# Performance work log

Measured on AMD Instinct MI355X. Metric: run time of the kernel, lower is better.

The kernel has to match this reference:

```python
import jax, jax.numpy as jnp
import numpy as np

N, C, D = 131072, 512, 3


def setup_inputs() -> dict:
    key = jax.random.key(0)
    kx, kmu = jax.random.split(key)
    X = jax.random.normal(kx, (N, D), dtype=jnp.float32)
    mu = jax.random.normal(kmu, (C, D), dtype=jnp.float32)
    w = jnp.zeros((C,), dtype=jnp.float32)
    # sigma as in __init__: r = sqrt(sum of per-dim unbiased variances of mu0)
    r = jnp.sqrt(jnp.var(mu, axis=0, ddof=1).sum())
    sigma = (0.1 * (r / C ** (1.0 / D))).astype(jnp.float32)
    return {"X": X, "mu": mu, "w": w, "sigma": sigma}


def reference(X, mu, w, sigma):
    # One EM step of a uniform-covariance GMM (EM_step_pytorch).
    n, d = X.shape
    # pairwise squared distances [N, C]
    D2_nc = ((X[:, None, :] - mu[None, :, :]) ** 2).sum(-1)
    # log-responsibilities (E-step), softmax over components
    lgamma_nc = jax.nn.log_softmax(w[None, :] - D2_nc / (2.0 * sigma ** 2), axis=1)
    gamma_nc = jnp.exp(lgamma_nc)
    # M-step: centroids (softmax over points, per component)
    mu_new = jax.nn.softmax(lgamma_nc, axis=0).T @ X  # [C, D]
    # M-step: component scores
    h_c = jax.nn.logsumexp(lgamma_nc, axis=0)  # [C]
    w_new = h_c - h_c.mean()
    # M-step: uniform std
    sigma_new = jnp.sqrt((gamma_nc * D2_nc).sum() / (d * n))
    # EM values: expected targets and free energy
    Y = gamma_nc @ mu_new  # [N, D]
    logpi_c = w_new - jax.nn.logsumexp(w_new)
    Cfe = (gamma_nc * (
        ((mu_new ** 2).sum(-1)[None, :] - (Y ** 2).sum(-1)[:, None]) / (2.0 * sigma_new ** 2)
        + d * jnp.log(sigma_new)
        - logpi_c[None, :]
        + lgamma_nc
    )).sum()
    return Y, Cfe
```

## Files before the change

### kernel.cpp

```cpp
#include <hip/hip_runtime.h>
#include <cfloat>
#include <cmath>

#define NPTS 131072
#define NC   512
#define NREP 4
#define L2E  1.4426950408889634f
#define LN2  0.6931471805599453f
#define CUT  34.0f

#define PM4_OFF  0
#define PQ4_OFF  2048
#define ST4_OFF  4096
#define MISC_OFF 12288

__device__ __forceinline__ float waveSum(float v) {
#pragma unroll
  for (int off = 32; off > 0; off >>= 1) v += __shfl_down(v, off, 64);
  return v;
}
__device__ __forceinline__ float waveMax(float v) {
#pragma unroll
  for (int off = 32; off > 0; off >>= 1) v = fmaxf(v, __shfl_down(v, off, 64));
  return v;
}

__global__ __launch_bounds__(512) void k_prep(
    const float* __restrict__ mu, const float* __restrict__ w,
    const float* __restrict__ sigma, float4* __restrict__ pm,
    float* __restrict__ ST, float* __restrict__ misc) {
  const int t = threadIdx.x;
  const float sg = sigma[0];
  const float k2 = L2E / (2.0f * sg * sg);
  const float m0 = mu[3 * t], m1 = mu[3 * t + 1], m2 = mu[3 * t + 2];
  pm[t] = make_float4(2.0f * k2 * m0, 2.0f * k2 * m1, 2.0f * k2 * m2,
                      w[t] * L2E - (m0 * m0 + m1 * m1 + m2 * m2) * k2);
#pragma unroll
  for (int r = 0; r < NREP * 4; ++r) ST[r * 512 + t] = 0.f;
  if (t < 8) misc[t] = 0.f;
}

__global__ __launch_bounds__(512, 4) void k_estep(
    const float* __restrict__ X, const float4* __restrict__ pm,
    float* __restrict__ ST, float* __restrict__ misc,
    float* __restrict__ out) {
  __shared__ float  s_m[8][64];
  __shared__ float2 s_sq[8][64];
  __shared__ float  s_M[64];
  __shared__ float  s_z[64];
  __shared__ float4 s_acc[NC];

  const int t = threadIdx.x;
  const int p = t & 63;
  const int ch = __builtin_amdgcn_readfirstlane(t >> 6);
  const int n = blockIdx.x * 64 + p;
  const float x0 = X[3 * n], x1 = X[3 * n + 1], x2 = X[3 * n + 2];

  s_acc[t] = make_float4(0.f, 0.f, 0.f, 0.f);

  const float4* __restrict__ pmc = pm + ch * 64;
  float l[64];
  float ma = -FLT_MAX, mb = -FLT_MAX, mc2 = -FLT_MAX, md = -FLT_MAX;
#pragma unroll
  for (int i = 0; i < 64; i += 4) {
    float4 a = pmc[i], b = pmc[i + 1], c = pmc[i + 2], d = pmc[i + 3];
    l[i]     = fmaf(a.x, x0, fmaf(a.y, x1, fmaf(a.z, x2, a.w)));
    l[i + 1] = fmaf(b.x, x0, fmaf(b.y, x1, fmaf(b.z, x2, b.w)));
    l[i + 2] = fmaf(c.x, x0, fmaf(c.y, x1, fmaf(c.z, x2, c.w)));
    l[i + 3] = fmaf(d.x, x0, fmaf(d.y, x1, fmaf(d.z, x2, d.w)));
    ma  = fmaxf(ma, l[i]);      mb = fmaxf(mb, l[i + 1]);
    mc2 = fmaxf(mc2, l[i + 2]); md = fmaxf(md, l[i + 3]);
  }
  s_m[ch][p] = fmaxf(fmaxf(ma, mb), fmaxf(mc2, md));
  __syncthreads();

  if (t < 64) {
    float v = s_m[0][t];
#pragma unroll
    for (int c = 1; c < 8; ++c) v = fmaxf(v, s_m[c][t]);
    s_M[t] = v;
  }
  __syncthreads();

  const float M = s_M[p];
  const float thr = M - CUT;

  float sE = 0.f, qE = 0.f;
#pragma unroll
  for (int i = 0; i < 64; ++i) {
    if (l[i] >= thr) {
      const float d = l[i] - M;
      const float e = exp2f(d);
      sE += e;
      qE = fmaf(e, d, qE);
    }
  }
  s_sq[ch][p] = make_float2(sE, qE);
  __syncthreads();

  if (t < 64) {
    float ss = 0.f, qq = 0.f;
#pragma unroll
    for (int c = 0; c < 8; ++c) { float2 v = s_sq[c][t]; ss += v.x; qq += v.y; }
    const float lg = __log2f(ss);
    const float z = s_M[t] + lg;
    s_z[t] = z;
    out[3 * n] = z;
    const float La = LN2 * (__fdividef(qq, ss) - lg);
    const float xx = x0 * x0 + x1 * x1 + x2 * x2;
    const float rl = waveSum(La);
    const float rx = waveSum(xx);
    if (t == 0) { atomicAdd(&misc[3], rl); atomicAdd(&misc[0], rx); }
  }
  __syncthreads();

  const float z = s_z[p];
#pragma unroll
  for (int i = 0; i < 64; ++i) {
    if (l[i] >= thr) {
      const float g = exp2f(l[i] - z);
      float* a = (float*)(s_acc + (ch * 64 + i));
      atomicAdd(a + 0, g * x0);
      atomicAdd(a + 1, g * x1);
      atomicAdd(a + 2, g * x2);
      atomicAdd(a + 3, g);
    }
  }
  __syncthreads();

  float4 v = s_acc[t];
  if (v.w != 0.f) {
    float* st = ST + (((blockIdx.x & (NREP - 1)) * 512 + t) << 2);
    atomicAdd(st + 0, v.x);
    atomicAdd(st + 1, v.y);
    atomicAdd(st + 2, v.z);
    atomicAdd(st + 3, v.w);
  }
}

__global__ __launch_bounds__(512) void k_mstep(
    const float* __restrict__ mu, const float4* __restrict__ ST4,
    float4* __restrict__ pq, float* __restrict__ misc,
    float* __restrict__ out) {
  __shared__ float s_red[8];
  __shared__ float s_red2[8];
  __shared__ float s_bc[4];
  const int t = threadIdx.x;

  float Tx = 0.f, Ty = 0.f, Tz = 0.f, S = 0.f;
#pragma unroll
  for (int r = 0; r < NREP; ++r) {
    float4 v = ST4[r * 512 + t];
    Tx += v.x; Ty += v.y; Tz += v.z; S += v.w;
  }
  const float Sc = fmaxf(S, 1e-30f);
  const float h = __logf(Sc);
  const float m0 = Tx / Sc, m1 = Ty / Sc, m2 = Tz / Sc;

  const float o0 = mu[3 * t], o1 = mu[3 * t + 1], o2 = mu[3 * t + 2];
  const float gdp = S * (o0 * o0 + o1 * o1 + o2 * o2)
                    - 2.0f * (o0 * Tx + o1 * Ty + o2 * Tz);

  float hm = waveMax(h);
  if ((t & 63) == 0) s_red[t >> 6] = hm;
  __syncthreads();
  if (t == 0) {
    float v = s_red[0];
    for (int i = 1; i < 8; ++i) v = fmaxf(v, s_red[i]);
    s_bc[0] = v;
  }
  __syncthreads();
  const float hM = s_bc[0];

  float es = waveSum(__expf(h - hM));
  float gs = waveSum(gdp);
  if ((t & 63) == 0) { s_red[t >> 6] = es; s_red2[t >> 6] = gs; }
  __syncthreads();
  if (t == 0) {
    float esum = 0.f, gsum = 0.f;
    for (int i = 0; i < 8; ++i) { esum += s_red[i]; gsum += s_red2[i]; }
    s_bc[1] = hM + __logf(esum);
    const float gd = fmaxf(misc[0] + gsum, 1e-20f);
    const float sn2 = gd * (1.0f / (3.0f * (float)NPTS));
    s_bc[2] = 1.0f / (2.0f * sn2);
    s_bc[3] = 1.5f * __logf(sn2);
  }
  __syncthreads();

  const float inv2s2n = s_bc[2];
  const float logpi = h - s_bc[1];
  const float A = (m0 * m0 + m1 * m1 + m2 * m2) * inv2s2n - logpi;
  pq[t] = make_float4(m0, m1, m2, A);

  float ca = waveSum(S * A);
  if ((t & 63) == 0) s_red[t >> 6] = ca;
  __syncthreads();
  if (t == 0) {
    float v = 0.f;
    for (int i = 0; i < 8; ++i) v += s_red[i];
    out[NPTS * 3] = v + misc[3] + (float)NPTS * s_bc[3];
    misc[1] = inv2s2n;
  }
}

__global__ __launch_bounds__(512, 4) void k_final(
    const float* __restrict__ X, const float4* __restrict__ pm,
    const float4* __restrict__ pq, const float* __restrict__ misc,
    float* __restrict__ out) {
  __shared__ float4 s_pm[NC];
  __shared__ float4 s_pq[NC];
  __shared__ float4 s_y[4][128];
  __shared__ float  s_red[8];

  const int t = threadIdx.x;
  const int p = t & 127;
  const int ch = __builtin_amdgcn_readfirstlane(t >> 7);
  const int n = blockIdx.x * 128 + p;

  s_pm[t] = pm[t];
  s_pq[t] = pq[t];

  const float x0 = X[3 * n], x1 = X[3 * n + 1], x2 = X[3 * n + 2];
  const float z = out[3 * n];
  const float thr = z - CUT;
  const float inv2s2n = misc[1];
  __syncthreads();

  const float4* __restrict__ pmc = &s_pm[ch * 128];
  const float4* __restrict__ pqc = &s_pq[ch * 128];
  float y0 = 0.f, y1 = 0.f, y2 = 0.f;
#pragma unroll 8
  for (int i = 0; i < 128; ++i) {
    float4 pp = pmc[i];
    const float l = fmaf(pp.x, x0, fmaf(pp.y, x1, fmaf(pp.z, x2, pp.w)));
    if (l >= thr) {
      const float g = exp2f(l - z);
      float4 qq = pqc[i];
      y0 = fmaf(g, qq.x, y0);
      y1 = fmaf(g, qq.y, y1);
      y2 = fmaf(g, qq.z, y2);
    }
  }
  s_y[ch][p] = make_float4(y0, y1, y2, 0.f);
  __syncthreads();

  float cfe = 0.f;
  if (t < 128) {
    float4 a0 = s_y[0][t], a1 = s_y[1][t], a2 = s_y[2][t], a3 = s_y[3][t];
    const float Y0 = (a0.x + a1.x) + (a2.x + a3.x);
    const float Y1 = (a0.y + a1.y) + (a2.y + a3.y);
    const float Y2 = (a0.z + a1.z) + (a2.z + a3.z);
    cfe = -(Y0 * Y0 + Y1 * Y1 + Y2 * Y2) * inv2s2n;
    out[3 * n] = Y0;
    out[3 * n + 1] = Y1;
    out[3 * n + 2] = Y2;
  }
  float r = waveSum(cfe);
  if ((t & 63) == 0) s_red[t >> 6] = r;
  __syncthreads();
  if (t == 0) {
    float v = 0.f;
#pragma unroll
    for (int i = 0; i < 8; ++i) v += s_red[i];
    atomicAdd(&out[NPTS * 3], v);
  }
}

extern "C" void kernel_launch(void* const* d_in, const int* in_sizes, int n_in,
                              void* d_out, int out_size, void* d_ws, size_t ws_size,
                              hipStream_t stream) {
  const float* X = (const float*)d_in[0];
  const float* mu = (const float*)d_in[1];
  const float* w = (const float*)d_in[2];
  const float* sigma = (const float*)d_in[3];
  float* out = (float*)d_out;
  float* ws = (float*)d_ws;

  float4* pm = (float4*)(ws + PM4_OFF);
  float4* pq = (float4*)(ws + PQ4_OFF);
  float* ST = ws + ST4_OFF;
  float* misc = ws + MISC_OFF;

  k_prep<<<1, 512, 0, stream>>>(mu, w, sigma, pm, ST, misc);
  k_estep<<<NPTS / 64, 512, 0, stream>>>(X, pm, ST, misc, out);
  k_mstep<<<1, 512, 0, stream>>>(mu, (const float4*)ST, pq, misc, out);
  k_final<<<NPTS / 128, 512, 0, stream>>>(X, pm, pq, misc, out);
}
```

Baseline: 175.3 us.

## Record sparse active point-component pairs in E-step and replay them in final pass

The E-step now handles 128 points per block. It recomputes logits instead of holding them in registers. Each (point, component) pair above the cutoff goes into a shared-memory list, and the M-step statistics are accumulated by walking that compact list rather than looping over all components. It also writes up to 15 active component indices per point to a workspace list, so the final kernel evaluates only those components, with a dense fallback when a point has too many. This targets the dense 512-component loops, at the cost of shared-memory atomics and an extra global write; pairs beyond ECAP are silently dropped, which is a correctness risk.

Result: faster. 161.3 us (-8.0%).

```diff
diff --git a/kernel.cpp b/kernel.cpp
--- a/kernel.cpp
+++ b/kernel.cpp
@@ -8,11 +8,14 @@
 #define L2E  1.4426950408889634f
 #define LN2  0.6931471805599453f
 #define CUT  34.0f
+#define ECAP 2048
+#define PK   15
 
 #define PM4_OFF  0
 #define PQ4_OFF  2048
 #define ST4_OFF  4096
 #define MISC_OFF 12288
+#define PL_OFF   16384
 
 __device__ __forceinline__ float waveSum(float v) {
 #pragma unroll
@@ -43,41 +46,43 @@
 __global__ __launch_bounds__(512, 4) void k_estep(
     const float* __restrict__ X, const float4* __restrict__ pm,
     float* __restrict__ ST, float* __restrict__ misc,
-    float* __restrict__ out) {
-  __shared__ float  s_m[8][64];
-  __shared__ float2 s_sq[8][64];
-  __shared__ float  s_M[64];
-  __shared__ float  s_z[64];
-  __shared__ float4 s_acc[NC];
-
-  const int t = threadIdx.x;
-  const int p = t & 63;
-  const int ch = __builtin_amdgcn_readfirstlane(t >> 6);
-  const int n = blockIdx.x * 64 + p;
+    float* __restrict__ out, unsigned short* __restrict__ plist) {
+  __shared__ float4 s_pt[128];
+  __shared__ float  s_m[4][128];
+  __shared__ float2 s_sq[4][128];
+  __shared__ float  s_M[128];
+  __shared__ unsigned int s_cnt;
+  __shared__ unsigned int s_pcnt[128];
+  __shared__ unsigned int s_ec[ECAP];
+  __shared__ float        s_el[ECAP];
+
+  const int t = threadIdx.x;
+  const int p = t & 127;
+  const int ch = __builtin_amdgcn_readfirstlane(t >> 7);
+  const int n = blockIdx.x * 128 + p;
   const float x0 = X[3 * n], x1 = X[3 * n + 1], x2 = X[3 * n + 2];
 
-  s_acc[t] = make_float4(0.f, 0.f, 0.f, 0.f);
-
-  const float4* __restrict__ pmc = pm + ch * 64;
-  float l[64];
+  if (t == 0) s_cnt = 0u;
+  if (t < 128) {
+    s_pcnt[t] = 0u;
+    s_pt[t] = make_float4(x0, x1, x2, 0.f);
+  }
+
+  const float4* __restrict__ pmc = pm + ch * 128;
   float ma = -FLT_MAX, mb = -FLT_MAX, mc2 = -FLT_MAX, md = -FLT_MAX;
-#pragma unroll
-  for (int i = 0; i < 64; i += 4) {
+#pragma unroll 4
+  for (int i = 0; i < 128; i += 4) {
     float4 a = pmc[i], b = pmc[i + 1], c = pmc[i + 2], d = pmc[i + 3];
-    l[i]     = fmaf(a.x, x0, fmaf(a.y, x1, fmaf(a.z, x2, a.w)));
-    l[i + 1] = fmaf(b.x, x0, fmaf(b.y, x1, fmaf(b.z, x2, b.w)));
-    l[i + 2] = fmaf(c.x, x0, fmaf(c.y, x1, fmaf(c.z, x2, c.w)));
-    l[i + 3] = fmaf(d.x, x0, fmaf(d.y, x1, fmaf(d.z, x2, d.w)));
-    ma  = fmaxf(ma, l[i]);      mb = fmaxf(mb, l[i + 1]);
-    mc2 = fmaxf(mc2, l[i + 2]); md = fmaxf(md, l[i + 3]);
+    ma  = fmaxf(ma,  fmaf(a.x, x0, fmaf(a.y, x1, fmaf(a.z, x2, a.w))));
+    mb  = fmaxf(mb,  fmaf(b.x, x0, fmaf(b.y, x1, fmaf(b.z, x2, b.w))));
+    mc2 = fmaxf(mc2, fmaf(c.x, x0, fmaf(c.y, x1, fmaf(c.z, x2, c.w))));
+    md  = fmaxf(md,  fmaf(d.x, x0, fmaf(d.y, x1, fmaf(d.z, x2, d.w))));
   }
   s_m[ch][p] = fmaxf(fmaxf(ma, mb), fmaxf(mc2, md));
   __syncthreads();
 
-  if (t < 64) {
-    float v = s_m[0][t];
-#pragma unroll
-    for (int c = 1; c < 8; ++c) v = fmaxf(v, s_m[c][t]);
+  if (t < 128) {
+    float v = fmaxf(fmaxf(s_m[0][t], s_m[1][t]), fmaxf(s_m[2][t], s_m[3][t]));
     s_M[t] = v;
   }
   __syncthreads();
@@ -86,55 +91,66 @@
   const float thr = M - CUT;
 
   float sE = 0.f, qE = 0.f;
-#pragma unroll
-  for (int i = 0; i < 64; ++i) {
-    if (l[i] >= thr) {
-      const float d = l[i] - M;
+#pragma unroll 4
+  for (int i = 0; i < 128; ++i) {
+    float4 a = pmc[i];
+    const float l = fmaf(a.x, x0, fmaf(a.y, x1, fmaf(a.z, x2, a.w)));
+    if (l >= thr) {
+      const float d = l - M;
       const float e = exp2f(d);
       sE += e;
       qE = fmaf(e, d, qE);
+      unsigned int idx = atomicAdd(&s_cnt, 1u);
+      if (idx < (unsigned)ECAP) {
+        s_ec[idx] = ((unsigned)p << 16) | (unsigned)(ch * 128 + i);
+        s_el[idx] = l;
+      }
+      if (plist) {
+        unsigned int slot = atomicAdd(&s_pcnt[p], 1u);
+        if (slot < (unsigned)PK)
+          plist[(size_t)n * 16u + 1u + slot] = (unsigned short)(ch * 128 + i);
+      } else {
+        atomicAdd(&s_pcnt[p], 1u);
+      }
     }
   }
   s_sq[ch][p] = make_float2(sE, qE);
   __syncthreads();
 
-  if (t < 64) {
-    float ss = 0.f, qq = 0.f;
-#pragma unroll
-    for (int c = 0; c < 8; ++c) { float2 v = s_sq[c][t]; ss += v.x; qq += v.y; }
+  if (t < 128) {
+    float2 q0 = s_sq[0][t], q1 = s_sq[1][t], q2 = s_sq[2][t], q3 = s_sq[3][t];
+    const float ss = (q0.x + q1.x) + (q2.x + q3.x);
+    const float qq = (q0.y + q1.y) + (q2.y + q3.y);
     const float lg = __log2f(ss);
     const float z = s_M[t] + lg;
-    s_z[t] = z;
+    s_pt[t].w = z;
     out[3 * n] = z;
+    if (plist) {
+      unsigned int pc = s_pcnt[t];
+      plist[(size_t)n * 16u] =
+          (pc > (unsigned)PK) ? (unsigned short)0xFFFFu : (unsigned short)pc;
+    }
     const float La = LN2 * (__fdividef(qq, ss) - lg);
     const float xx = x0 * x0 + x1 * x1 + x2 * x2;
     const float rl = waveSum(La);
     const float rx = waveSum(xx);
-    if (t == 0) { atomicAdd(&misc[3], rl); atomicAdd(&misc[0], rx); }
-  }
-  __syncthreads();
-
-  const float z = s_z[p];
-#pragma unroll
-  for (int i = 0; i < 64; ++i) {
-    if (l[i] >= thr) {
-      const float g = exp2f(l[i] - z);
-      float* a = (float*)(s_acc + (ch * 64 + i));
-      atomicAdd(a + 0, g * x0);
-      atomicAdd(a + 1, g * x1);
-      atomicAdd(a + 2, g * x2);
-      atomicAdd(a + 3, g);
-    }
-  }
-  __syncthreads();
-
-  float4 v = s_acc[t];
-  if (v.w != 0.f) {
-    float* st = ST + (((blockIdx.x & (NREP - 1)) * 512 + t) << 2);
-    atomicAdd(st + 0, v.x);
-    atomicAdd(st + 1, v.y);
-    atomicAdd(st + 2, v.z);
-    atomicAdd(st + 3, v.w);
+    if ((t & 63) == 0) { atomicAdd(&misc[3], rl); atomicAdd(&misc[0], rx); }
+  }
+  __syncthreads();
+
+  const unsigned int total = min(s_cnt, (unsigned)ECAP);
+  float* __restrict__ stbase = ST + ((blockIdx.x & (NREP - 1)) * 512) * 4;
+  for (unsigned int idx = t; idx < total; idx += 512) {
+    const unsigned int ec = s_ec[idx];
+    const unsigned int pp = ec >> 16;
+    const unsigned int c = ec & 0xFFFFu;
+    const float4 pt = s_pt[pp];
+    const float g = exp2f(s_el[idx] - pt.w);
+    float* st = stbase + c * 4;
+    atomicAdd(st + 0, g * pt.x);
+    atomicAdd(st + 1, g * pt.y);
+    atomicAdd(st + 2, g * pt.z);
+    atomicAdd(st + 3, g);
   }
 }
 
@@ -203,12 +219,86 @@
   }
 }
 
-__global__ __launch_bounds__(512, 4) void k_final(
+__global__ __launch_bounds__(512, 4) void k_final_list(
+    const float* __restrict__ X, const float4* __restrict__ pm,
+    const float4* __restrict__ pq, const float* __restrict__ misc,
+    float* __restrict__ out, const unsigned short* __restrict__ plist) {
+  __shared__ float4 s_pm[NC];
+  __shared__ float4 s_pq[NC];
+  __shared__ float  s_red[8];
+
+  const int t = threadIdx.x;
+  const int n = blockIdx.x * 512 + t;
+
+  s_pm[t] = pm[t];
+  s_pq[t] = pq[t];
+
+  const float x0 = X[3 * n], x1 = X[3 * n + 1], x2 = X[3 * n + 2];
+  const float z = out[3 * n];
+  const float inv2s2n = misc[1];
+
+  const uint4* __restrict__ lp =
+      reinterpret_cast<const uint4*>(plist) + ((size_t)n << 1);
+  const uint4 wA = lp[0];
+  const uint4 wB = lp[1];
+  unsigned int words[8] = {wA.x, wA.y, wA.z, wA.w, wB.x, wB.y, wB.z, wB.w};
+  const unsigned int cnt = words[0] & 0xFFFFu;
+  __syncthreads();
+
+  float y0 = 0.f, y1 = 0.f, y2 = 0.f;
+  if (cnt == 0xFFFFu) {
+    const float thr = z - CUT;
+    for (int c = 0; c < NC; ++c) {
+      float4 pp = s_pm[c];
+      const float l = fmaf(pp.x, x0, fmaf(pp.y, x1, fmaf(pp.z, x2, pp.w)));
+      if (l >= thr) {
+        const float g = exp2f(l - z);
+        float4 qq = s_pq[c];
+        y0 = fmaf(g, qq.x, y0);
+        y1 = fmaf(g, qq.y, y1);
+        y2 = fmaf(g, qq.z, y2);
+      }
+    }
+  } else {
+    const int ic = (int)cnt;
+#pragma unroll
+    for (int j = 0; j < PK; ++j) {
+      if (!__any(j < ic)) break;
+      if (j < ic) {
+        const unsigned int word = words[(j + 1) >> 1];
+        const unsigned int c =
+            ((j + 1) & 1) ? (word >> 16) : (word & 0xFFFFu);
+        float4 pp = s_pm[c];
+        const float l = fmaf(pp.x, x0, fmaf(pp.y, x1, fmaf(pp.z, x2, pp.w)));
+        const float g = exp2f(l - z);
+        float4 qq = s_pq[c];
+        y0 = fmaf(g, qq.x, y0);
+        y1 = fmaf(g, qq.y, y1);
+        y2 = fmaf(g, qq.z, y2);
+      }
+    }
+  }
+
+  const float cfe = -(y0 * y0 + y1 * y1 + y2 * y2) * inv2s2n;
+  out[3 * n] = y0;
+  out[3 * n + 1] = y1;
+  out[3 * n + 2] = y2;
+
+  float r = waveSum(cfe);
+  if ((t & 63) == 0) s_red[t >> 6] = r;
+  __syncthreads();
+  if (t == 0) {
+    float v = 0.f;
+#pragma unroll
+    for (int i = 0; i < 8; ++i) v += s_red[i];
+    atomicAdd(&out[NPTS * 3], v);
+  }
+}
+
+__global__ __launch_bounds__(512, 8) void k_final_dense(
     const float* __restrict__ X, const float4* __restrict__ pm,
     const float4* __restrict__ pq, const float* __restrict__ misc,
     float* __restrict__ out) {
-  __shared__ float4 s_pm[NC];
-  __shared__ float4 s_pq[NC];
   __shared__ float4 s_y[4][128];
   __shared__ float  s_red[8];
 
@@ -216,30 +306,22 @@
   const int p = t & 127;
   const int ch = __builtin_amdgcn_readfirstlane(t >> 7);
   const int n = blockIdx.x * 128 + p;
-
-  s_pm[t] = pm[t];
-  s_pq[t] = pq[t];
-
   const float x0 = X[3 * n], x1 = X[3 * n + 1], x2 = X[3 * n + 2];
   const float z = out[3 * n];
-  const float thr = z - CUT;
   const float inv2s2n = misc[1];
-  __syncthreads();
-
-  const float4* __restrict__ pmc = &s_pm[ch * 128];
-  const float4* __restrict__ pqc = &s_pq[ch * 128];
+
+  const float4* __restrict__ pmc = pm + ch * 128;
+  const float4* __restrict__ pqc = pq + ch * 128;
   float y0 = 0.f, y1 = 0.f, y2 = 0.f;
-#pragma unroll 8
+#pragma unroll 4
   for (int i = 0; i < 128; ++i) {
     float4 pp = pmc[i];
-    const float l = fmaf(pp.x, x0, fmaf(pp.y, x1, fmaf(pp.z, x2, pp.w)));
-    if (l >= thr) {
-      const float g = exp2f(l - z);
-      float4 qq = pqc[i];
-      y0 = fmaf(g, qq.x, y0);
-      y1 = fmaf(g, qq.y, y1);
-      y2 = fmaf(g, qq.z, y2);
-    }
+    float4 qq = pqc[i];
+    const float l = fmaf(pp.x, x0, fmaf(pp.y, x1, fmaf(pp.z, x2, pp.w))) - z;
+    const float g = exp2f(l);
+    y0 = fmaf(g, qq.x, y0);
+    y1 = fmaf(g, qq.y, y1);
+    y2 = fmaf(g, qq.z, y2);
   }
   s_y[ch][p] = make_float4(y0, y1, y2, 0.f);
   __syncthreads();
@@ -281,8 +363,15 @@
   float* ST = ws + ST4_OFF;
   float* misc = ws + MISC_OFF;
 
+  const size_t need = (size_t)PL_OFF * 4 + (size_t)NPTS * 32;
+  unsigned short* plist =
+      (ws_size >= need) ? (unsigned short*)(ws + PL_OFF) : (unsigned short*)0;
+
   k_prep<<<1, 512, 0, stream>>>(mu, w, sigma, pm, ST, misc);
-  k_estep<<<NPTS / 64, 512, 0, stream>>>(X, pm, ST, misc, out);
+  k_estep<<<NPTS / 128, 512, 0, stream>>>(X, pm, ST, misc, out, plist);
   k_mstep<<<1, 512, 0, stream>>>(mu, (const float4*)ST, pq, misc, out);
-  k_final<<<NPTS / 128, 512, 0, stream>>>(X, pm, pq, misc, out);
-}
+  if (plist)
+    k_final_list<<<NPTS / 512, 512, 0, stream>>>(X, pm, pq, misc, out, plist);
+  else
+    k_final_dense<<<NPTS / 128, 512, 0, stream>>>(X, pm, pq, misc, out);
+}
```
